# Kernel tuning notes

Measured on AMD Instinct MI355X. Metric: run time of the kernel, lower is better.

## Reference

```python
import jax, jax.numpy as jnp
import numpy as np


def setup_inputs() -> dict:
    key = jax.random.key(0)
    k1, k2, k3, k4, k5 = jax.random.split(key, 5)
    B, C, H, W = 16, 256, 32, 32
    G = 4
    gd = C // G
    x = jax.random.normal(k1, (B, C, H, W), dtype=jnp.float32)
    # grouped 1x1 convs == per-group [gd, gd] linear maps (torch weight (C, C//G, 1, 1))
    s = 1.0 / np.sqrt(gd)
    wq = jax.random.normal(k2, (G, gd, gd), dtype=jnp.float32) * s
    wk = jax.random.normal(k3, (G, gd, gd), dtype=jnp.float32) * s
    wv = jax.random.normal(k4, (G, gd, gd), dtype=jnp.float32) * s
    wo = jax.random.normal(k5, (C, C), dtype=jnp.float32) * (1.0 / np.sqrt(C))
    return {"x": x, "wq": wq, "wk": wk, "wv": wv, "wo": wo}


def reference(x, wq, wk, wv, wo):
    B, C, H, W = x.shape
    G, gd = wq.shape[0], wq.shape[1]
    N = H * W
    xg = x.reshape(B, G, gd, N)  # split channels into groups, flatten spatial
    # grouped 1x1 conv projections: out[d] = sum_c w[d,c] * x[c] per group
    Q = jnp.einsum('bgcn,gdc->bgdn', xg, wq)
    K = jnp.einsum('bgcn,gdc->bgdn', xg, wk)
    V = jnp.einsum('bgcn,gdc->bgdn', xg, wv)
    scale = 1.0 / (float(gd) ** 0.5)
    # scores: Q^T K over channel dim -> [B, G, N, N]
    scores = jnp.einsum('bgdn,bgdm->bgnm', Q, K) * scale
    attn = jax.nn.softmax(scores, axis=-1)
    # out[d, n] = sum_m attn[n, m] * V[d, m]  (== (attn @ V^T)^T in torch code)
    out = jnp.einsum('bgnm,bgdm->bgdn', attn, V)
    out = out.reshape(B, C, H, W)
    # out_proj: dense 1x1 conv over all channels
    return jnp.einsum('bchw,dc->bdhw', out, wo)
```

## Files before the change

### kernel.cpp

```cpp
#include <hip/hip_runtime.h>
#include <hip/hip_bf16.h>


typedef __bf16 bf16x8 __attribute__((ext_vector_type(8)));
typedef short s16x8 __attribute__((ext_vector_type(8)));
typedef float f32x4 __attribute__((ext_vector_type(4)));

__device__ __forceinline__ unsigned short f2b(float f) {
  unsigned int u = __builtin_bit_cast(unsigned int, f);
  u += 0x7fffu + ((u >> 16) & 1u);
  return (unsigned short)(u >> 16);
}
__device__ __forceinline__ unsigned short bf16u(float f) {
  return __builtin_bit_cast(unsigned short, __float2bfloat16(f));
}
__device__ __forceinline__ f32x4 mfma16(s16x8 a, s16x8 b, f32x4 c) {
  return __builtin_amdgcn_mfma_f32_16x16x32_bf16(
      __builtin_bit_cast(bf16x8, a), __builtin_bit_cast(bf16x8, b), c, 0, 0, 0);
}
__device__ __forceinline__ void gload16(const void* g, void* l) {
  __builtin_amdgcn_global_load_lds((const __attribute__((address_space(1))) void*)g,
                                   (__attribute__((address_space(3))) void*)l, 16, 0, 0);
}
__device__ __forceinline__ void stage8k(const unsigned short* g, short* l, int wid, int lane) {
  gload16(g + wid * 1024 + lane * 8,       l + wid * 1024);
  gload16(g + wid * 1024 + 512 + lane * 8, l + wid * 1024 + 512);
}

__global__ void prep_kernel(const float* __restrict__ wq, const float* __restrict__ wk,
                            const float* __restrict__ wv, const float* __restrict__ wo,
                            unsigned short* __restrict__ Mts, unsigned short* __restrict__ Ub) {
  int id = blockIdx.x * 256 + threadIdx.x;
  if (blockIdx.x < 64) {
    int g = id >> 12, e = (id >> 6) & 63, c = id & 63;
    const float* q = wq + g * 4096;
    const float* k = wk + g * 4096;
    float acc = 0.f;
    for (int d = 0; d < 64; ++d) acc += q[d * 64 + c] * k[d * 64 + e];
    Mts[g * 4096 + e * 64 + (c ^ ((e & 7) << 3))] = f2b(acc * 0.125f * 1.4426950408889634f);
  } else {
    int i = id - 16384;
    int o = i >> 8, gc = i & 255, g = gc >> 6, c = gc & 63;
    const float* v = wv + g * 4096;
    const float* w = wo + o * 256 + g * 64;
    float acc = 0.f;
    for (int d = 0; d < 64; ++d) acc += w[d] * v[d * 64 + c];
    Ub[i] = f2b(acc);
  }
}

__global__ __launch_bounds__(256) void cvt_kernel(const float* __restrict__ x,
                                                  unsigned short* __restrict__ XbT,
                                                  unsigned short* __restrict__ Xbs) {
  __shared__ __align__(16) short T[64][72];
  const int chunk = blockIdx.x;
  const int head = chunk >> 4;
  const int t0 = (chunk & 15) * 64;
  const int tid = threadIdx.x;
  const float* Xg = x + (size_t)head * 65536 + t0;
  for (int i = 0; i < 4; ++i) {
    int row = i * 16 + (tid >> 4);
    int col = (tid & 15) * 4;
    float4 v = *(const float4*)(Xg + (size_t)row * 1024 + col);
    ushort4 s4 = make_ushort4(f2b(v.x), f2b(v.y), f2b(v.z), f2b(v.w));
    *(ushort4*)&T[row][col] = s4;
  }
  __syncthreads();
  unsigned short* oT = XbT + (size_t)chunk * 4096;
  unsigned short* oC = Xbs + (size_t)chunk * 4096;
  for (int p = 0; p < 2; ++p) {
    int idx = p * 256 + tid;
    int rr = idx >> 3, j = idx & 7;
    int sb = (j ^ (rr & 7)) * 8;
    unsigned short w[8];
    for (int i = 0; i < 8; ++i) w[i] = (unsigned short)T[sb + i][rr];
    *(s16x8*)(oT + rr * 64 + j * 8) = *(s16x8*)w;
    s16x8 rv = *(const s16x8*)&T[rr][sb];
    *(s16x8*)(oC + rr * 64 + j * 8) = rv;
  }
}

__global__ __launch_bounds__(256, 3)
void attn_kernel(const unsigned short* __restrict__ XbT, const unsigned short* __restrict__ Xbs,
                 const unsigned short* __restrict__ Mts, unsigned short* __restrict__ Ast) {
  __shared__ __align__(16) short XtB[2][4096];
  __shared__ __align__(16) short XcB[2][4096];
  __shared__ __align__(16) short Pb[128 * 72];

  const int f = blockIdx.x;
  const int bg = (f & 7) + ((f >> 6) << 3);
  const int n0 = ((f >> 3) & 7) * 128;
  const int tid = threadIdx.x;
  const int wid = tid >> 6;
  const int lane = tid & 63;
  const int l15 = lane & 15, l4 = lane >> 4;
  const int swz = (l15 & 7) << 3;
  const unsigned short* xtg = XbT + (size_t)bg * 65536;
  const unsigned short* xcg = Xbs + (size_t)bg * 65536;
  short* Ps = Pb;

  stage8k(Mts + (bg & 3) * 4096, &XcB[0][0], wid, lane);
  stage8k(xtg + (size_t)(n0 >> 6) * 4096, &XtB[0][0], wid, lane);
  stage8k(xtg + (size_t)((n0 >> 6) + 1) * 4096, &XtB[1][0], wid, lane);
  __syncthreads();

  s16x8 qpB[2][2];
  {
    s16x8 bm[4][2];
    for (int eb = 0; eb < 4; ++eb)
      for (int kc = 0; kc < 2; ++kc)
        bm[eb][kc] = *(const s16x8*)&XcB[0][(eb * 16 + l15) * 64 + ((kc * 32 + l4 * 8) ^ swz)];
    for (int nt = 0; nt < 2; ++nt) {
      int q = wid * 32 + nt * 16;
      int h = q >> 6, rl = (q & 63) + l15;
      int rsw = ((rl & 7) << 3);
      s16x8 a0 = *(const s16x8*)&XtB[h][rl * 64 + ((l4 * 8) ^ rsw)];
      s16x8 a1 = *(const s16x8*)&XtB[h][rl * 64 + ((32 + l4 * 8) ^ rsw)];
      for (int eb = 0; eb < 4; ++eb) {
        f32x4 acc = {0.f, 0.f, 0.f, 0.f};
        acc = mfma16(a0, bm[eb][0], acc);
        acc = mfma16(a1, bm[eb][1], acc);
        for (int r = 0; r < 4; ++r)
          Ps[(q + 4 * l4 + r) * 72 + eb * 16 + l15] = (short)bf16u(acc[r]);
      }
    }
  }
  asm volatile("s_waitcnt lgkmcnt(0)" ::: "memory");
  __builtin_amdgcn_sched_barrier(0);
  for (int nt = 0; nt < 2; ++nt)
    for (int kc = 0; kc < 2; ++kc)
      qpB[nt][kc] = *(const s16x8*)&Ps[(wid * 32 + nt * 16 + l15) * 72 + kc * 32 + l4 * 8];
  __syncthreads();

  stage8k(xtg, &XtB[0][0], wid, lane);
  stage8k(xcg, &XcB[0][0], wid, lane);
  __syncthreads();

  float rowSp[2] = {0.f, 0.f};
  f32x4 acc[2][4];
  for (int nt = 0; nt < 2; ++nt)
    for (int cb = 0; cb < 4; ++cb) acc[nt][cb] = (f32x4){0.f, 0.f, 0.f, 0.f};

#define CHUNK_BODY(cur, k)                                                              \
  {                                                                                     \
    if ((k) < 15) {                                                                     \
      stage8k(xtg + (size_t)((k) + 1) * 4096, &XtB[(cur) ^ 1][0], wid, lane);           \
      stage8k(xcg + (size_t)((k) + 1) * 4096, &XcB[(cur) ^ 1][0], wid, lane);           \
    }                                                                                   \
    s16x8 xt[4][2], ax[4][2];                                                           \
    for (int mb = 0; mb < 4; ++mb) {                                                    \
      int rm = mb * 16 + l15;                                                           \
      xt[mb][0] = *(const s16x8*)&XtB[cur][rm * 64 + ((l4 * 8) ^ swz)];                 \
      xt[mb][1] = *(const s16x8*)&XtB[cur][rm * 64 + ((32 + l4 * 8) ^ swz)];            \
      ax[mb][0] = *(const s16x8*)&XcB[cur][rm * 64 + ((l4 * 8) ^ swz)];                 \
      ax[mb][1] = *(const s16x8*)&XcB[cur][rm * 64 + ((32 + l4 * 8) ^ swz)];            \
    }                                                                                   \
    f32x4 s[2][4];                                                                      \
    for (int nt = 0; nt < 2; ++nt)                                                      \
      for (int mb = 0; mb < 4; ++mb) {                                                  \
        f32x4 a = {0.f, 0.f, 0.f, 0.f};                                                 \
        a = mfma16(xt[mb][0], qpB[nt][0], a);                                           \
        a = mfma16(xt[mb][1], qpB[nt][1], a);                                           \
        s[nt][mb] = a;                                                                  \
      }                                                                                 \
    for (int nt = 0; nt < 2; ++nt) {                                                    \
      const int prow = (wid * 32 + nt * 16 + l15) * 72;                                 \
      float ps = 0.f;                                                                   \
      for (int mb = 0; mb < 4; ++mb) {                                                  \
        float p0 = __builtin_amdgcn_exp2f(s[nt][mb][0]);                                \
        float p1 = __builtin_amdgcn_exp2f(s[nt][mb][1]);                                \
        float p2 = __builtin_amdgcn_exp2f(s[nt][mb][2]);                                \
        float p3 = __builtin_amdgcn_exp2f(s[nt][mb][3]);                                \
        ps += (p0 + p1) + (p2 + p3);                                                    \
        ushort4 pk = make_ushort4(bf16u(p0), bf16u(p1), bf16u(p2), bf16u(p3));          \
        *(ushort4*)&Ps[prow + mb * 16 + l4 * 4] = pk;                                   \
      }                                                                                 \
      rowSp[nt] += ps;                                                                  \
    }                                                                                   \
    asm volatile("s_waitcnt lgkmcnt(0)" ::: "memory");                                  \
    __builtin_amdgcn_sched_barrier(0);                                                  \
    for (int nt = 0; nt < 2; ++nt) {                                                    \
      const int prow = (wid * 32 + nt * 16 + l15) * 72;                                 \
      s16x8 pb0 = *(const s16x8*)&Ps[prow + l4 * 8];                                    \
      s16x8 pb1 = *(const s16x8*)&Ps[prow + 32 + l4 * 8];                               \
      for (int cb = 0; cb < 4; ++cb) {                                                  \
        acc[nt][cb] = mfma16(ax[cb][0], pb0, acc[nt][cb]);                              \
        acc[nt][cb] = mfma16(ax[cb][1], pb1, acc[nt][cb]);                              \
      }                                                                                 \
    }                                                                                   \
    __syncthreads();                                                                    \
  }

  for (int k = 0; k < 16; k += 2) {
    CHUNK_BODY(0, k)
    CHUNK_BODY(1, k + 1)
  }
#undef CHUNK_BODY

  const int b = bg >> 2, g = bg & 3;
  for (int nt = 0; nt < 2; ++nt) {
    float t = rowSp[nt];
    t += __shfl_xor(t, 16, 64);
    t += __shfl_xor(t, 32, 64);
    float inv = 1.f / t;
    int n = n0 + wid * 32 + nt * 16 + l15;
    unsigned short* Ag = Ast + ((size_t)(b * 1024 + n)) * 256 + g * 64;
    for (int cb = 0; cb < 4; ++cb) {
      f32x4 v = acc[nt][cb];
      ushort4 pk = make_ushort4(bf16u(v[0] * inv), bf16u(v[1] * inv),
                                bf16u(v[2] * inv), bf16u(v[3] * inv));
      *(ushort4*)(Ag + cb * 16 + l4 * 4) = pk;
    }
  }
}

__global__ __launch_bounds__(256, 2)
void proj_kernel(const unsigned short* __restrict__ Ub, const unsigned short* __restrict__ Ast,
                 float* __restrict__ out) {
  const int b = blockIdx.z;
  const int o0 = blockIdx.y * 128;
  const int n0 = blockIdx.x * 128;
  const int tid = threadIdx.x;
  const int wid = tid >> 6;
  const int lane = tid & 63;
  const int l15 = lane & 15, l4 = lane >> 4;
  const int ow = o0 + (wid & 1) * 64;
  const int nw = n0 + (wid >> 1) * 64;
  const unsigned short* A_ = Ast + ((size_t)b * 1024 + nw) * 256;

  f32x4 acc[4][4];
  for (int i = 0; i < 4; ++i)
    for (int j = 0; j < 4; ++j) acc[i][j] = (f32x4){0.f, 0.f, 0.f, 0.f};

  for (int kc = 0; kc < 8; ++kc) {
    s16x8 af[4], bfr[4];
    for (int ob = 0; ob < 4; ++ob)
      af[ob] = *(const s16x8*)(Ub + (size_t)(ow + ob * 16 + l15) * 256 + kc * 32 + l4 * 8);
    for (int nb = 0; nb < 4; ++nb)
      bfr[nb] = *(const s16x8*)(A_ + (size_t)(nb * 16 + l15) * 256 + kc * 32 + l4 * 8);
    for (int ob = 0; ob < 4; ++ob)
      for (int nb = 0; nb < 4; ++nb)
        acc[ob][nb] = mfma16(af[ob], bfr[nb], acc[ob][nb]);
  }
  float* O = out + ((size_t)b * 256 + ow) * 1024 + nw;
  for (int ob = 0; ob < 4; ++ob)
    for (int r = 0; r < 4; ++r)
      for (int nb = 0; nb < 4; ++nb)
        O[(size_t)(ob * 16 + l4 * 4 + r) * 1024 + nb * 16 + l15] = acc[ob][nb][r];
}

extern "C" void kernel_launch(void* const* d_in, const int* in_sizes, int n_in,
                              void* d_out, int out_size, void* d_ws, size_t ws_size,
                              hipStream_t stream) {
  const float* x  = (const float*)d_in[0];
  const float* wq = (const float*)d_in[1];
  const float* wk = (const float*)d_in[2];
  const float* wv = (const float*)d_in[3];
  const float* wo = (const float*)d_in[4];
  float* out = (float*)d_out;
  char* ws = (char*)d_ws;
  unsigned short* XbT = (unsigned short*)(ws);
  unsigned short* Xbs = (unsigned short*)(ws + 8388608);
  unsigned short* Mts = (unsigned short*)(ws + 16777216);
  unsigned short* Ub  = (unsigned short*)(ws + 16777216 + 32768);
  unsigned short* Ast = (unsigned short*)(ws + 16777216 + 163840);

  prep_kernel<<<320, 256, 0, stream>>>(wq, wk, wv, wo, Mts, Ub);
  cvt_kernel<<<1024, 256, 0, stream>>>(x, XbT, Xbs);
  attn_kernel<<<512, 256, 0, stream>>>(XbT, Xbs, Mts, Ast);
  proj_kernel<<<dim3(8, 2, 16), 256, 0, stream>>>(Ub, Ast, out);
}
```

Measured before the change: 58.01 us.

## Triple-buffer attention chunk loads with vmcnt waits and remap cvt blocks across XCDs

The attention main loop moves from double buffering with a trailing __syncthreads to a three-deep LDS ring. Loads are prefetched two chunks ahead, and each step starts with an explicit s_waitcnt vmcnt plus a barrier, so global-to-LDS traffic overlaps more compute. This grows LDS use and lowers launch bounds from 3 to 2 blocks per CU, which may cut latency hiding from occupancy. Separately, the conversion kernel remaps block IDs so that neighbouring heads land on the same XCD, matching the attention kernel's block mapping for L2 locality.

Result: faster. 55.70 us (-4.0%).

```diff
diff --git a/kernel.cpp b/kernel.cpp
--- a/kernel.cpp
+++ b/kernel.cpp
@@ -53,9 +53,13 @@
                                                   unsigned short* __restrict__ XbT,
                                                   unsigned short* __restrict__ Xbs) {
   __shared__ __align__(16) short T[64][72];
-  const int chunk = blockIdx.x;
-  const int head = chunk >> 4;
-  const int t0 = (chunk & 15) * 64;
+  const int f = blockIdx.x;
+  const int xcd = f & 7;
+  const int idx = f >> 3;
+  const int head = ((idx & 7) << 3) | xcd;
+  const int tile = idx >> 3;
+  const int chunk = head * 16 + tile;
+  const int t0 = tile * 64;
   const int tid = threadIdx.x;
   const float* Xg = x + (size_t)head * 65536 + t0;
   for (int i = 0; i < 4; ++i) {
@@ -69,8 +73,8 @@
   unsigned short* oT = XbT + (size_t)chunk * 4096;
   unsigned short* oC = Xbs + (size_t)chunk * 4096;
   for (int p = 0; p < 2; ++p) {
-    int idx = p * 256 + tid;
-    int rr = idx >> 3, j = idx & 7;
+    int idx2 = p * 256 + tid;
+    int rr = idx2 >> 3, j = idx2 & 7;
     int sb = (j ^ (rr & 7)) * 8;
     unsigned short w[8];
     for (int i = 0; i < 8; ++i) w[i] = (unsigned short)T[sb + i][rr];
@@ -80,11 +84,11 @@
   }
 }
 
-__global__ __launch_bounds__(256, 3)
+__global__ __launch_bounds__(256, 2)
 void attn_kernel(const unsigned short* __restrict__ XbT, const unsigned short* __restrict__ Xbs,
                  const unsigned short* __restrict__ Mts, unsigned short* __restrict__ Ast) {
-  __shared__ __align__(16) short XtB[2][4096];
-  __shared__ __align__(16) short XcB[2][4096];
+  __shared__ __align__(16) short XtB[3][4096];
+  __shared__ __align__(16) short XcB[3][4096];
   __shared__ __align__(16) short Pb[128 * 72];
 
   const int f = blockIdx.x;
@@ -132,28 +136,33 @@
       qpB[nt][kc] = *(const s16x8*)&Ps[(wid * 32 + nt * 16 + l15) * 72 + kc * 32 + l4 * 8];
   __syncthreads();
 
-  stage8k(xtg, &XtB[0][0], wid, lane);
-  stage8k(xcg, &XcB[0][0], wid, lane);
-  __syncthreads();
+  stage8k(xtg,        &XtB[0][0], wid, lane);
+  stage8k(xcg,        &XcB[0][0], wid, lane);
+  stage8k(xtg + 4096, &XtB[1][0], wid, lane);
+  stage8k(xcg + 4096, &XcB[1][0], wid, lane);
 
   float rowSp[2] = {0.f, 0.f};
   f32x4 acc[2][4];
   for (int nt = 0; nt < 2; ++nt)
     for (int cb = 0; cb < 4; ++cb) acc[nt][cb] = (f32x4){0.f, 0.f, 0.f, 0.f};
 
-#define CHUNK_BODY(cur, k)                                                              \
+#define STEP(K, VMC)                                                                    \
   {                                                                                     \
-    if ((k) < 15) {                                                                     \
-      stage8k(xtg + (size_t)((k) + 1) * 4096, &XtB[(cur) ^ 1][0], wid, lane);           \
-      stage8k(xcg + (size_t)((k) + 1) * 4096, &XcB[(cur) ^ 1][0], wid, lane);           \
-    }                                                                                   \
+    asm volatile("s_waitcnt vmcnt(" VMC ")" ::: "memory");                              \
+    __builtin_amdgcn_s_barrier();                                                       \
+    __builtin_amdgcn_sched_barrier(0);                                                  \
+    if ((K) < 14) {                                                                     \
+      stage8k(xtg + (size_t)((K) + 2) * 4096, &XtB[((K) + 2) % 3][0], wid, lane);       \
+      stage8k(xcg + (size_t)((K) + 2) * 4096, &XcB[((K) + 2) % 3][0], wid, lane);       \
+    }                                                                                   \
+    const int cs = (K) % 3;                                                             \
     s16x8 xt[4][2], ax[4][2];                                                           \
     for (int mb = 0; mb < 4; ++mb) {                                                    \
       int rm = mb * 16 + l15;                                                           \
-      xt[mb][0] = *(const s16x8*)&XtB[cur][rm * 64 + ((l4 * 8) ^ swz)];                 \
-      xt[mb][1] = *(const s16x8*)&XtB[cur][rm * 64 + ((32 + l4 * 8) ^ swz)];            \
-      ax[mb][0] = *(const s16x8*)&XcB[cur][rm * 64 + ((l4 * 8) ^ swz)];                 \
-      ax[mb][1] = *(const s16x8*)&XcB[cur][rm * 64 + ((32 + l4 * 8) ^ swz)];            \
+      xt[mb][0] = *(const s16x8*)&XtB[cs][rm * 64 + ((l4 * 8) ^ swz)];                  \
+      xt[mb][1] = *(const s16x8*)&XtB[cs][rm * 64 + ((32 + l4 * 8) ^ swz)];             \
+      ax[mb][0] = *(const s16x8*)&XcB[cs][rm * 64 + ((l4 * 8) ^ swz)];                  \
+      ax[mb][1] = *(const s16x8*)&XcB[cs][rm * 64 + ((32 + l4 * 8) ^ swz)];             \
     }                                                                                   \
     f32x4 s[2][4];                                                                      \
     for (int nt = 0; nt < 2; ++nt)                                                      \
@@ -188,14 +197,13 @@
         acc[nt][cb] = mfma16(ax[cb][1], pb1, acc[nt][cb]);                              \
       }                                                                                 \
     }                                                                                   \
-    __syncthreads();                                                                    \
-  }
-
-  for (int k = 0; k < 16; k += 2) {
-    CHUNK_BODY(0, k)
-    CHUNK_BODY(1, k + 1)
-  }
-#undef CHUNK_BODY
+  }
+
+  STEP(0, "4")  STEP(1, "4")  STEP(2, "4")  STEP(3, "4")
+  STEP(4, "4")  STEP(5, "4")  STEP(6, "4")  STEP(7, "4")
+  STEP(8, "4")  STEP(9, "4")  STEP(10, "4") STEP(11, "4")
+  STEP(12, "4") STEP(13, "4") STEP(14, "4") STEP(15, "0")
+#undef STEP
 
   const int b = bg >> 2, g = bg & 3;
   for (int nt = 0; nt < 2; ++nt) {
```
